# Performance work log

Measured on AMD Instinct MI355X. Metric: run time of the kernel, lower is better.

## Reference

```python
import jax, jax.numpy as jnp
import numpy as np

N_NODES = 100000
D = 128
N_EDGES = 640000


def _spmm(edge_index, w, x, n):
    # out[i] = sum over edges (i<-j): w * x[j]
    src, dst = edge_index[0], edge_index[1]
    return jax.ops.segment_sum(w[:, None] * x[dst], src, num_segments=n)


def setup_inputs() -> dict:
    key = jax.random.key(0)
    ks = jax.random.split(key, 8)
    inp = {
        "index_vectors": jax.random.normal(ks[0], (N_NODES, D), dtype=jnp.float32),
        "edge_index1": jax.random.randint(ks[1], (2, N_EDGES), 0, N_NODES, dtype=jnp.int64),
        "w1": jnp.ones((N_EDGES,), dtype=jnp.float32),
        "edge_index2": jax.random.randint(ks[2], (2, N_EDGES), 0, N_NODES, dtype=jnp.int64),
        "w2": jnp.ones((N_EDGES,), dtype=jnp.float32),
        "edge_index3": jax.random.randint(ks[3], (2, N_EDGES), 0, N_NODES, dtype=jnp.int64),
        "w3": jnp.ones((N_EDGES,), dtype=jnp.float32),
        "zeroth": jax.random.uniform(ks[4], (1, 1), dtype=jnp.float32),
        "fst": jax.random.uniform(ks[5], (1, 1), dtype=jnp.float32),
        "snd": jax.random.uniform(ks[6], (1, 1), dtype=jnp.float32),
        "trd": jax.random.uniform(ks[7], (1, 1), dtype=jnp.float32),
    }
    return inp


def reference(index_vectors, edge_index1, w1, edge_index2, w2, edge_index3, w3,
              zeroth, fst, snd, trd):
    n = index_vectors.shape[0]
    # hop-1 context: A @ x
    fst_ctx = _spmm(edge_index1, w1, index_vectors, n)
    # hop-2 context: A^2 @ roll(x, 1, axis=1)   (permute_vecs=True)
    snd_ctx = _spmm(edge_index2, w2, jnp.roll(index_vectors, 1, axis=1), n)
    # hop-3 context: A^3 @ roll(x, 2, axis=1)
    trd_ctx = _spmm(edge_index3, w3, jnp.roll(index_vectors, 2, axis=1), n)

    # relu-normalized scalar order weights (get_orders)
    r0, r1, r2, r3 = (jax.nn.relu(zeroth), jax.nn.relu(fst),
                      jax.nn.relu(snd), jax.nn.relu(trd))
    tot = r0 + r1 + r2 + r3 + 1e-6
    r0, r1, r2, r3 = r0 / tot, r1 / tot, r2 / tot, r3 / tot

    # use_sign=False -> plain weighted combination
    return r0 * index_vectors + r1 * fst_ctx + r2 * snd_ctx + r3 * trd_ctx
```

## Files before the change

kernel.cpp:

```cpp
#include <hip/hip_runtime.h>

#define N_NODES 100000
#define D 128
#define N_EDGES 640000
#define TOT_EDGES (3 * N_EDGES)

#define NB   1024
#define NPB  98
#define BCAP 2304
#define RPT  9
#define OVF_CAP 16384
#define NKEY 512

#define EPBA 2560
#define SETBLKA (N_EDGES / EPBA)
#define BLKA (3 * SETBLKA)
#define EPT2 (EPBA / 256)

#define CAST_BLOCKS ((N_NODES * D / 4 + 255) / 256)

#define WS_OVFCNT 0
#define WS_CNT    64
#define WS_TOT    3072064
#define WS_OVF    3076160
#define WS_TMP    3338304
#define WS_OFFS   22212672
#define WS_CNTS   22612672
#define WS_XB     23012672
#define WS_TOTAL_FAST 48612672

#ifndef __has_builtin
#define __has_builtin(x) 0
#endif
#if __has_builtin(__builtin_amdgcn_alignbit)
#define ALIGN16(hi, lo) __builtin_amdgcn_alignbit((hi), (lo), 16)
#else
#define ALIGN16(hi, lo) (((hi) << 16) | ((lo) >> 16))
#endif

__device__ __forceinline__ void load_r(const float* z0, const float* z1,
                                       const float* z2, const float* z3,
                                       float& r0, float& r1, float& r2, float& r3) {
    r0 = fmaxf(z0[0], 0.0f);
    r1 = fmaxf(z1[0], 0.0f);
    r2 = fmaxf(z2[0], 0.0f);
    r3 = fmaxf(z3[0], 0.0f);
    float inv = 1.0f / (r0 + r1 + r2 + r3 + 1e-6f);
    r0 *= inv; r1 *= inv; r2 *= inv; r3 *= inv;
}

__device__ __forceinline__ unsigned short bf16rn(float f) {
    unsigned int u = __float_as_uint(f);
    u += 0x7FFFu + ((u >> 16) & 1u);
    return (unsigned short)(u >> 16);
}

__global__ __launch_bounds__(256) void cast_kernel(const float* __restrict__ x,
                                                   ushort* __restrict__ xb) {
    int i = blockIdx.x * 256 + threadIdx.x;
    if (i >= N_NODES * D / 4) return;
    float4 v = ((const float4*)x)[i];
    ushort4 h;
    h.x = bf16rn(v.x); h.y = bf16rn(v.y); h.z = bf16rn(v.z); h.w = bf16rn(v.w);
    ((ushort4*)xb)[i] = h;
}

__global__ __launch_bounds__(256) void histA_kernel(
        const int* __restrict__ ei1, const int* __restrict__ ei2,
        const int* __restrict__ ei3, int* __restrict__ counts) {
    __shared__ int h[NB];
    int t = threadIdx.x;
    int blk = blockIdx.x;
    for (int i = t; i < NB; i += 256) h[i] = 0;
    __syncthreads();
    int set = blk / SETBLKA;
    int e0  = (blk - set * SETBLKA) * EPBA;
    const int* ei = (set == 0) ? ei1 : (set == 1) ? ei2 : ei3;
    for (int i = t; i < EPBA; i += 256) {
        atomicAdd(&h[ei[e0 + i] / NPB], 1);
    }
    __syncthreads();
    for (int i = t; i < NB; i += 256) counts[blk * NB + i] = h[i];
}

__global__ __launch_bounds__(256) void scanA_kernel(int* __restrict__ counts,
                                                    int* __restrict__ totals) {
    int b = blockIdx.x * 256 + threadIdx.x;
    int run = 0;
    for (int blk = 0; blk < BLKA; ++blk) {
        int c = counts[blk * NB + b];
        counts[blk * NB + b] = run;
        run += c;
    }
    totals[b] = run;
}

__global__ __launch_bounds__(256) void placeA_kernel(
        const int* __restrict__ ei1, const float* __restrict__ w1,
        const int* __restrict__ ei2, const float* __restrict__ w2,
        const int* __restrict__ ei3, const float* __restrict__ w3,
        const float* __restrict__ z0, const float* __restrict__ z1,
        const float* __restrict__ z2, const float* __restrict__ z3,
        const int* __restrict__ bbase,
        int* __restrict__ ovf_count, int4* __restrict__ ovf,
        int2* __restrict__ tmp) {
    __shared__ int bb[NB];
    __shared__ int h[NB];
    __shared__ int ts[256];
    __shared__ int2 srec[EPBA];
    __shared__ int gx[EPBA];

    int t = threadIdx.x;
    int blk = blockIdx.x;
    for (int i = t; i < NB; i += 256) { bb[i] = bbase[blk * NB + i]; h[i] = 0; }
    __syncthreads();

    int set = blk / SETBLKA;
    int e0  = (blk - set * SETBLKA) * EPBA;
    const int* ei;  const float* w;  float rk;
    float r0, r1, r2, r3;
    load_r(z0, z1, z2, z3, r0, r1, r2, r3);
    if      (set == 0) { ei = ei1; w = w1; rk = r1; }
    else if (set == 1) { ei = ei2; w = w2; rk = r2; }
    else               { ei = ei3; w = w3; rk = r3; }

    int bkt[EPT2], rnk[EPT2], lcl[EPT2], dstv[EPT2];
    float scv[EPT2];
#pragma unroll
    for (int k = 0; k < EPT2; ++k) {
        int idx = e0 + t + k * 256;
        int src = ei[idx];
        dstv[k] = ei[N_EDGES + idx];
        scv[k]  = rk * w[idx];
        int b = src / NPB;
        bkt[k] = b;
        lcl[k] = src - b * NPB;
        rnk[k] = atomicAdd(&h[b], 1);
    }
    __syncthreads();

    int loc[4];
    int tot = 0;
#pragma unroll
    for (int k = 0; k < 4; ++k) { loc[k] = tot; tot += h[4 * t + k]; }
    ts[t] = tot;
    __syncthreads();
    for (int off = 1; off < 256; off <<= 1) {
        int v = (t >= off) ? ts[t - off] : 0;
        __syncthreads();
        ts[t] += v;
        __syncthreads();
    }
    int tb = ts[t] - tot;
    __syncthreads();
#pragma unroll
    for (int k = 0; k < 4; ++k) h[4 * t + k] = tb + loc[k];
    __syncthreads();

#pragma unroll
    for (int k = 0; k < EPT2; ++k) {
        int b = bkt[k];
        int s = h[b] + rnk[k];
        int rx = dstv[k] | (set << 17) | (lcl[k] << 19);
        srec[s] = make_int2(rx, __float_as_int(scv[k]));
        int p = bb[b] + rnk[k];
        if (p < BCAP) {
            gx[s] = b * BCAP + p;
        } else {
            gx[s] = -1;
            int o = atomicAdd(ovf_count, 1);
            if (o < OVF_CAP) ovf[o] = make_int4(b * NPB + lcl[k],
                                               dstv[k] | (set << 17),
                                               __float_as_int(scv[k]), 0);
        }
    }
    __syncthreads();

    for (int s = t; s < EPBA; s += 256) {
        int g = gx[s];
        if (g >= 0) tmp[g] = srec[s];
    }
}

__global__ __launch_bounds__(256) void binB_kernel(
        const int* __restrict__ totals, int2* __restrict__ tmp,
        int* __restrict__ offs, int* __restrict__ cnts) {
    __shared__ int dH[NKEY];
    __shared__ int ts[256];
    __shared__ int cur[NKEY];
    __shared__ int nb[NPB + 1];
    int b = blockIdx.x;
    int t = threadIdx.x;
    int n = totals[b];
    if (n > BCAP) n = BCAP;

    int mrx[RPT], mry[RPT];
#pragma unroll
    for (int k = 0; k < RPT; ++k) {
        int i = t + k * 256;
        if (i < n) { int2 r = tmp[(size_t)b * BCAP + i]; mrx[k] = r.x; mry[k] = r.y; }
        else       { mrx[k] = -1; mry[k] = 0; }
    }

    dH[t] = 0; dH[t + 256] = 0;
    __syncthreads();
#pragma unroll
    for (int k = 0; k < RPT; ++k) {
        if (mrx[k] != -1) {
            int key = (((mrx[k] >> 19) & 0x7F) << 2) | ((mrx[k] >> 17) & 3);
            atomicAdd(&dH[key], 1);
        }
    }
    __syncthreads();

    int k0 = dH[2 * t], k1 = dH[2 * t + 1];
    int tot = k0 + k1;
    ts[t] = tot;
    __syncthreads();
    for (int off = 1; off < 256; off <<= 1) {
        int v = (t >= off) ? ts[t - off] : 0;
        __syncthreads();
        ts[t] += v;
        __syncthreads();
    }
    int tb = ts[t] - tot;
    cur[2 * t]     = tb;
    cur[2 * t + 1] = tb + k0;
    __syncthreads();

    if (t <= NPB) nb[t] = (t < NPB) ? cur[t << 2] : n;
    __syncthreads();

#pragma unroll
    for (int k = 0; k < RPT; ++k) {
        if (mrx[k] != -1) {
            int key = (((mrx[k] >> 19) & 0x7F) << 2) | ((mrx[k] >> 17) & 3);
            int pos = atomicAdd(&cur[key], 1);
            tmp[(size_t)b * BCAP + pos] = make_int2(mrx[k], mry[k]);
        }
    }

    if (t < NPB) {
        int node = b * NPB + t;
        if (node < N_NODES) {
            offs[node] = b * BCAP + nb[t];
            cnts[node] = nb[t + 1] - nb[t];
        }
    }
}

#define GB_ACCUM(RX, RY)                                                       \
    {                                                                          \
        const uint4* rowp = (const uint4*)(xb + (size_t)((RX) & 0x1FFFF) * D); \
        uint4 v = rowp[l16];                                                   \
        int sh = ((RX) >> 17) & 3;                                             \
        float sc = __int_as_float(RY);                                         \
        unsigned int pw = (unsigned int)__shfl((int)v.w, prevq);               \
        unsigned int s1x = ALIGN16(v.x, pw);                                   \
        unsigned int s1y = ALIGN16(v.y, v.x);                                  \
        unsigned int s1z = ALIGN16(v.z, v.y);                                  \
        unsigned int s1w = ALIGN16(v.w, v.z);                                  \
        unsigned int u0 = (sh == 0) ? v.x : (sh == 1) ? s1x : pw;              \
        unsigned int u1 = (sh == 0) ? v.y : (sh == 1) ? s1y : v.x;             \
        unsigned int u2 = (sh == 0) ? v.z : (sh == 1) ? s1z : v.y;             \
        unsigned int u3 = (sh == 0) ? v.w : (sh == 1) ? s1w : v.z;             \
        acc0 += sc * __uint_as_float(u0 << 16);                                \
        acc1 += sc * __uint_as_float(u0 & 0xFFFF0000u);                        \
        acc2 += sc * __uint_as_float(u1 << 16);                                \
        acc3 += sc * __uint_as_float(u1 & 0xFFFF0000u);                        \
        acc4 += sc * __uint_as_float(u2 << 16);                                \
        acc5 += sc * __uint_as_float(u2 & 0xFFFF0000u);                        \
        acc6 += sc * __uint_as_float(u3 << 16);                                \
        acc7 += sc * __uint_as_float(u3 & 0xFFFF0000u);                        \
    }

__global__ __launch_bounds__(256) void gatherb_kernel(
        const float* __restrict__ x, const ushort* __restrict__ xb,
        const int* __restrict__ offs, const int* __restrict__ cnts,
        const int2* __restrict__ recs,
        const float* __restrict__ z0, const float* __restrict__ z1,
        const float* __restrict__ z2, const float* __restrict__ z3,
        float* __restrict__ out) {
    int wid  = (blockIdx.x * blockDim.x + threadIdx.x) >> 6;
    int lane = threadIdx.x & 63;
    if (wid >= N_NODES) return;

    float r0, r1, r2, r3;
    load_r(z0, z1, z2, z3, r0, r1, r2, r3);

    int qt    = lane >> 4;
    int l16   = lane & 15;
    int prevq = (qt << 4) | ((l16 + 15) & 15);

    int beg   = offs[wid];
    int count = cnts[wid];
    int cnt64 = (count < 64) ? count : 64;

    int mrx = 0, mry = 0;
    if (lane < cnt64) { int2 rec = recs[beg + lane]; mrx = rec.x; mry = rec.y; }

    float acc0 = 0.f, acc1 = 0.f, acc2 = 0.f, acc3 = 0.f;
    float acc4 = 0.f, acc5 = 0.f, acc6 = 0.f, acc7 = 0.f;

    for (int j = 0; j < cnt64; j += 4) {
        int srcl = j + qt;
        int rx = __shfl(mrx, srcl);
        int ry = __shfl(mry, srcl);
        GB_ACCUM(rx, ry)
    }
    for (int q = 64; q < count; q += 4) {
        int qq = q + qt;
        int rx = 0, ry = 0;
        if (qq < count) { int2 rec = recs[beg + qq]; rx = rec.x; ry = rec.y; }
        GB_ACCUM(rx, ry)
    }

    acc0 += __shfl_xor(acc0, 16); acc0 += __shfl_xor(acc0, 32);
    acc1 += __shfl_xor(acc1, 16); acc1 += __shfl_xor(acc1, 32);
    acc2 += __shfl_xor(acc2, 16); acc2 += __shfl_xor(acc2, 32);
    acc3 += __shfl_xor(acc3, 16); acc3 += __shfl_xor(acc3, 32);
    acc4 += __shfl_xor(acc4, 16); acc4 += __shfl_xor(acc4, 32);
    acc5 += __shfl_xor(acc5, 16); acc5 += __shfl_xor(acc5, 32);
    acc6 += __shfl_xor(acc6, 16); acc6 += __shfl_xor(acc6, 32);
    acc7 += __shfl_xor(acc7, 16); acc7 += __shfl_xor(acc7, 32);

    if (lane < 16) {
        const float4* xr = (const float4*)(x + (size_t)wid * D);
        float4 xlo = xr[2 * l16];
        float4 xhi = xr[2 * l16 + 1];
        float4 olo, ohi;
        olo.x = r0 * xlo.x + acc0;
        olo.y = r0 * xlo.y + acc1;
        olo.z = r0 * xlo.z + acc2;
        olo.w = r0 * xlo.w + acc3;
        ohi.x = r0 * xhi.x + acc4;
        ohi.y = r0 * xhi.y + acc5;
        ohi.z = r0 * xhi.z + acc6;
        ohi.w = r0 * xhi.w + acc7;
        float4* op = (float4*)(out + (size_t)wid * D);
        op[2 * l16]     = olo;
        op[2 * l16 + 1] = ohi;
    }
}

__global__ void ovf_kernel(const float* __restrict__ x,
                           const int* __restrict__ ovf_count,
                           const int4* __restrict__ ovf,
                           float* __restrict__ out) {
    int total_waves = (gridDim.x * blockDim.x) >> 6;
    int gw   = (blockIdx.x * blockDim.x + threadIdx.x) >> 6;
    int lane = threadIdx.x & 63;
    int n = *ovf_count;
    if (n > OVF_CAP) n = OVF_CAP;
    for (int r = gw; r < n; r += total_waves) {
        int4 rec = ovf[r];
        int src = rec.x;
        int dst = rec.y & 0x1FFFF;
        int sh  = (rec.y >> 17) & 3;
        float sc = __int_as_float(rec.z);
        const float* xr = x + (size_t)dst * D;
        float* orow = out + (size_t)src * D;
        int c0 = 2 * lane, c1 = 2 * lane + 1;
        atomicAdd(&orow[c0], sc * xr[(c0 - sh) & 127]);
        atomicAdd(&orow[c1], sc * xr[(c1 - sh) & 127]);
    }
}

#define SCAN_BLOCKS ((N_NODES + 255) / 256)
#define WS_COUNTS   0
#define WS_OFFSETS  400000
#define WS_CURSORS  800008
#define WS_BSUM     1200008
#define WS_BPRE     1201576
#define WS_RECS     1203144
#define WS_NEEDED_MID (WS_RECS + (size_t)TOT_EDGES * 8)

__global__ void hist_kernel(const int* __restrict__ ei1, const int* __restrict__ ei2,
                            const int* __restrict__ ei3, int* __restrict__ counts) {
    int e = blockIdx.x * blockDim.x + threadIdx.x;
    if (e >= TOT_EDGES) return;
    int set = e / N_EDGES;
    int idx = e - set * N_EDGES;
    const int* ei = (set == 0) ? ei1 : (set == 1) ? ei2 : ei3;
    atomicAdd(&counts[ei[idx]], 1);
}

__global__ void scan1_kernel(const int* __restrict__ counts,
                             int* __restrict__ offsets, int* __restrict__ bsum) {
    __shared__ int s[256];
    int t = threadIdx.x;
    int i = blockIdx.x * 256 + t;
    int v = (i < N_NODES) ? counts[i] : 0;
    s[t] = v;
    __syncthreads();
    for (int off = 1; off < 256; off <<= 1) {
        int u = (t >= off) ? s[t - off] : 0;
        __syncthreads();
        s[t] += u;
        __syncthreads();
    }
    if (i < N_NODES) offsets[i] = s[t] - v;
    if (t == 255) bsum[blockIdx.x] = s[255];
}

__global__ void scan2_kernel(const int* __restrict__ bsum, int* __restrict__ bpre) {
    __shared__ int s[512];
    int t = threadIdx.x;
    int v = (t < SCAN_BLOCKS) ? bsum[t] : 0;
    s[t] = v;
    __syncthreads();
    for (int off = 1; off < 512; off <<= 1) {
        int u = (t >= off) ? s[t - off] : 0;
        __syncthreads();
        s[t] += u;
        __syncthreads();
    }
    if (t < SCAN_BLOCKS) bpre[t] = s[t] - v;
}

__global__ void scan3_kernel(int* __restrict__ offsets, const int* __restrict__ bpre,
                             int* __restrict__ cursors) {
    int i = blockIdx.x * 256 + threadIdx.x;
    if (i < N_NODES) {
        int v = offsets[i] + bpre[blockIdx.x];
        offsets[i] = v;
        cursors[i] = v;
    }
    if (i == 0) offsets[N_NODES] = TOT_EDGES;
}

__global__ void fill_kernel(const int* __restrict__ ei1, const float* __restrict__ w1,
                            const int* __restrict__ ei2, const float* __restrict__ w2,
                            const int* __restrict__ ei3, const float* __restrict__ w3,
                            const float* __restrict__ z0, const float* __restrict__ z1,
                            const float* __restrict__ z2, const float* __restrict__ z3,
                            int* __restrict__ cursors, int2* __restrict__ recs) {
    int e = blockIdx.x * blockDim.x + threadIdx.x;
    if (e >= TOT_EDGES) return;
    int set = e / N_EDGES;
    int idx = e - set * N_EDGES;
    const int* ei;  const float* w;
    if      (set == 0) { ei = ei1; w = w1; }
    else if (set == 1) { ei = ei2; w = w2; }
    else               { ei = ei3; w = w3; }
    float r0, r1, r2, r3;
    load_r(z0, z1, z2, z3, r0, r1, r2, r3);
    float rk = (set == 0) ? r1 : (set == 1) ? r2 : r3;
    int src = ei[idx];
    int dst = ei[N_EDGES + idx];
    float scale = rk * w[idx];
    int pos = atomicAdd(&cursors[src], 1);
    recs[pos] = make_int2(dst | (set << 17), __float_as_int(scale));
}

__global__ void gatherd_kernel(const float* __restrict__ x,
                               const int* __restrict__ offsets,
                               const int2* __restrict__ recs,
                               const float* __restrict__ z0, const float* __restrict__ z1,
                               const float* __restrict__ z2, const float* __restrict__ z3,
                               float* __restrict__ out) {
    int wid  = (blockIdx.x * blockDim.x + threadIdx.x) >> 6;
    int lane = threadIdx.x & 63;
    if (wid >= N_NODES) return;
    float r0, r1, r2, r3;
    load_r(z0, z1, z2, z3, r0, r1, r2, r3);
    float2 xv = ((const float2*)(x + (size_t)wid * D))[lane];
    int beg = offsets[wid];
    int end = offsets[wid + 1];
    float2 a0 = {0.f, 0.f}, a1 = {0.f, 0.f}, a2 = {0.f, 0.f};
    for (int j = beg; j < end; ++j) {
        int2 rec = recs[j];
        float2 v = ((const float2*)(x + (size_t)(rec.x & 0x1FFFF) * D))[lane];
        int sh = (rec.x >> 17) & 3;
        float sc = __int_as_float(rec.y);
        if      (sh == 0) { a0.x += sc * v.x; a0.y += sc * v.y; }
        else if (sh == 1) { a1.x += sc * v.x; a1.y += sc * v.y; }
        else               { a2.x += sc * v.x; a2.y += sc * v.y; }
    }
    int prev = (lane + 63) & 63;
    float r1y = __shfl(a1.y, prev);
    float r2x = __shfl(a2.x, prev);
    float r2y = __shfl(a2.y, prev);
    float2 o;
    o.x = r0 * xv.x + a0.x + r1y  + r2x;
    o.y = r0 * xv.y + a0.y + a1.x + r2y;
    ((float2*)(out + (size_t)wid * D))[lane] = o;
}

extern "C" void kernel_launch(void* const* d_in, const int* in_sizes, int n_in,
                              void* d_out, int out_size, void* d_ws, size_t ws_size,
                              hipStream_t stream) {
    const float* x   = (const float*)d_in[0];
    const int*   ei1 = (const int*)  d_in[1];
    const float* w1  = (const float*)d_in[2];
    const int*   ei2 = (const int*)  d_in[3];
    const float* w2  = (const float*)d_in[4];
    const int*   ei3 = (const int*)  d_in[5];
    const float* w3  = (const float*)d_in[6];
    const float* z0  = (const float*)d_in[7];
    const float* z1  = (const float*)d_in[8];
    const float* z2  = (const float*)d_in[9];
    const float* z3  = (const float*)d_in[10];
    float* out = (float*)d_out;
    char* wsc = (char*)d_ws;

    if (ws_size >= WS_TOTAL_FAST) {
        int*    ovf_count = (int*)   (wsc + WS_OVFCNT);
        int*    counts    = (int*)   (wsc + WS_CNT);
        int*    totals    = (int*)   (wsc + WS_TOT);
        int4*   ovf       = (int4*)  (wsc + WS_OVF);
        int2*   tmp       = (int2*)  (wsc + WS_TMP);
        int*    offs      = (int*)   (wsc + WS_OFFS);
        int*    cnts      = (int*)   (wsc + WS_CNTS);
        ushort* xb        = (ushort*)(wsc + WS_XB);

        hipMemsetAsync(wsc, 0, 64, stream);
        cast_kernel<<<CAST_BLOCKS, 256, 0, stream>>>(x, xb);
        histA_kernel<<<BLKA, 256, 0, stream>>>(ei1, ei2, ei3, counts);
        scanA_kernel<<<4, 256, 0, stream>>>(counts, totals);
        placeA_kernel<<<BLKA, 256, 0, stream>>>(ei1, w1, ei2, w2, ei3, w3,
                                                z0, z1, z2, z3,
                                                counts, ovf_count, ovf, tmp);
        binB_kernel<<<NB, 256, 0, stream>>>(totals, tmp, offs, cnts);
        gatherb_kernel<<<(N_NODES * 64 + 255) / 256, 256, 0, stream>>>(
            x, xb, offs, cnts, tmp, z0, z1, z2, z3, out);
        ovf_kernel<<<128, 256, 0, stream>>>(x, ovf_count, ovf, out);
    } else {
        int*  counts  = (int*) (wsc + WS_COUNTS);
        int*  offsets = (int*) (wsc + WS_OFFSETS);
        int*  cursors = (int*) (wsc + WS_CURSORS);
        int*  bsum    = (int*) (wsc + WS_BSUM);
        int*  bpre    = (int*) (wsc + WS_BPRE);
        int2* recs    = (int2*)(wsc + WS_RECS);

        hipMemsetAsync(counts, 0, N_NODES * sizeof(int), stream);
        hist_kernel<<<TOT_EDGES / 256, 256, 0, stream>>>(ei1, ei2, ei3, counts);
        scan1_kernel<<<SCAN_BLOCKS, 256, 0, stream>>>(counts, offsets, bsum);
        scan2_kernel<<<1, 512, 0, stream>>>(bsum, bpre);
        scan3_kernel<<<SCAN_BLOCKS, 256, 0, stream>>>(offsets, bpre, cursors);
        fill_kernel<<<TOT_EDGES / 256, 256, 0, stream>>>(ei1, w1, ei2, w2, ei3, w3,
                                                         z0, z1, z2, z3, cursors, recs);
        gatherd_kernel<<<(N_NODES * 64 + 255) / 256, 256, 0, stream>>>(x, offsets, recs,
                                                                       z0, z1, z2, z3, out);
    }
}
```

Before: 296.6 us.

## Replace histogram+scan bucket placement with global atomic cursors and fuse cast

Removes the separate histogram and column-scan kernels. Each placement block now reserves its per-bucket slots by calling atomicAdd on padded global cursors, and the bf16 cast of x runs as extra blocks inside the same launch. This cuts two kernel launches, one full pass over the edge indices and the serial 750-block scan. In exchange, the order of records inside each bucket is no longer deterministic, and there are 1024 contended global atomics per block. The workspace memset grows to cover the cursors.

```diff
diff --git a/kernel.cpp b/kernel.cpp
--- a/kernel.cpp
+++ b/kernel.cpp
@@ -20,14 +20,13 @@
 #define CAST_BLOCKS ((N_NODES * D / 4 + 255) / 256)
 
 #define WS_OVFCNT 0
-#define WS_CNT    64
-#define WS_TOT    3072064
-#define WS_OVF    3076160
-#define WS_TMP    3338304
-#define WS_OFFS   22212672
-#define WS_CNTS   22612672
-#define WS_XB     23012672
-#define WS_TOTAL_FAST 48612672
+#define WS_BCUR   64
+#define WS_OVF    65600
+#define WS_TMP    327744
+#define WS_OFFS   19202112
+#define WS_CNTS   19602112
+#define WS_XB     20002112
+#define WS_TOTAL_FAST 45602112
 
 #ifndef __has_builtin
 #define __has_builtin(x) 0
@@ -55,55 +54,26 @@
     return (unsigned short)(u >> 16);
 }
 
-__global__ __launch_bounds__(256) void cast_kernel(const float* __restrict__ x,
-                                                   ushort* __restrict__ xb) {
-    int i = blockIdx.x * 256 + threadIdx.x;
-    if (i >= N_NODES * D / 4) return;
-    float4 v = ((const float4*)x)[i];
-    ushort4 h;
-    h.x = bf16rn(v.x); h.y = bf16rn(v.y); h.z = bf16rn(v.z); h.w = bf16rn(v.w);
-    ((ushort4*)xb)[i] = h;
-}
-
-__global__ __launch_bounds__(256) void histA_kernel(
-        const int* __restrict__ ei1, const int* __restrict__ ei2,
-        const int* __restrict__ ei3, int* __restrict__ counts) {
-    __shared__ int h[NB];
-    int t = threadIdx.x;
-    int blk = blockIdx.x;
-    for (int i = t; i < NB; i += 256) h[i] = 0;
-    __syncthreads();
-    int set = blk / SETBLKA;
-    int e0  = (blk - set * SETBLKA) * EPBA;
-    const int* ei = (set == 0) ? ei1 : (set == 1) ? ei2 : ei3;
-    for (int i = t; i < EPBA; i += 256) {
-        atomicAdd(&h[ei[e0 + i] / NPB], 1);
-    }
-    __syncthreads();
-    for (int i = t; i < NB; i += 256) counts[blk * NB + i] = h[i];
-}
-
-__global__ __launch_bounds__(256) void scanA_kernel(int* __restrict__ counts,
-                                                    int* __restrict__ totals) {
-    int b = blockIdx.x * 256 + threadIdx.x;
-    int run = 0;
-    for (int blk = 0; blk < BLKA; ++blk) {
-        int c = counts[blk * NB + b];
-        counts[blk * NB + b] = run;
-        run += c;
-    }
-    totals[b] = run;
-}
-
-__global__ __launch_bounds__(256) void placeA_kernel(
+__global__ __launch_bounds__(256) void prep_kernel(
+        const float* __restrict__ x, ushort* __restrict__ xb,
         const int* __restrict__ ei1, const float* __restrict__ w1,
         const int* __restrict__ ei2, const float* __restrict__ w2,
         const int* __restrict__ ei3, const float* __restrict__ w3,
         const float* __restrict__ z0, const float* __restrict__ z1,
         const float* __restrict__ z2, const float* __restrict__ z3,
-        const int* __restrict__ bbase,
-        int* __restrict__ ovf_count, int4* __restrict__ ovf,
-        int2* __restrict__ tmp) {
+        int* __restrict__ bcur, int* __restrict__ ovf_count,
+        int4* __restrict__ ovf, int2* __restrict__ tmp) {
+    if (blockIdx.x >= BLKA) {
+        int i = (blockIdx.x - BLKA) * 256 + threadIdx.x;
+        if (i < N_NODES * D / 4) {
+            float4 v = ((const float4*)x)[i];
+            ushort4 h4;
+            h4.x = bf16rn(v.x); h4.y = bf16rn(v.y);
+            h4.z = bf16rn(v.z); h4.w = bf16rn(v.w);
+            ((ushort4*)xb)[i] = h4;
+        }
+        return;
+    }
     __shared__ int bb[NB];
     __shared__ int h[NB];
     __shared__ int ts[256];
@@ -112,14 +82,15 @@
 
     int t = threadIdx.x;
     int blk = blockIdx.x;
-    for (int i = t; i < NB; i += 256) { bb[i] = bbase[blk * NB + i]; h[i] = 0; }
-    __syncthreads();
+    for (int i = t; i < NB; i += 256) h[i] = 0;
+    __syncthreads();
+
+    float r0, r1, r2, r3;
+    load_r(z0, z1, z2, z3, r0, r1, r2, r3);
 
     int set = blk / SETBLKA;
     int e0  = (blk - set * SETBLKA) * EPBA;
     const int* ei;  const float* w;  float rk;
-    float r0, r1, r2, r3;
-    load_r(z0, z1, z2, z3, r0, r1, r2, r3);
     if      (set == 0) { ei = ei1; w = w1; rk = r1; }
     else if (set == 1) { ei = ei2; w = w2; rk = r2; }
     else               { ei = ei3; w = w3; rk = r3; }
@@ -143,6 +114,10 @@
     int tot = 0;
 #pragma unroll
     for (int k = 0; k < 4; ++k) { loc[k] = tot; tot += h[4 * t + k]; }
+    for (int i = t; i < NB; i += 256) {
+        int c = h[i];
+        bb[i] = c ? atomicAdd(&bcur[i * 16], c) : 0;
+    }
     ts[t] = tot;
     __syncthreads();
     for (int off = 1; off < 256; off <<= 1) {
@@ -183,7 +158,7 @@
 }
 
 __global__ __launch_bounds__(256) void binB_kernel(
-        const int* __restrict__ totals, int2* __restrict__ tmp,
+        const int* __restrict__ bcur, int2* __restrict__ tmp,
         int* __restrict__ offs, int* __restrict__ cnts) {
     __shared__ int dH[NKEY];
     __shared__ int ts[256];
@@ -191,7 +166,7 @@
     __shared__ int nb[NPB + 1];
     int b = blockIdx.x;
     int t = threadIdx.x;
-    int n = totals[b];
+    int n = bcur[b * 16];
     if (n > BCAP) n = BCAP;
 
     int mrx[RPT], mry[RPT];
@@ -506,22 +481,18 @@
 
     if (ws_size >= WS_TOTAL_FAST) {
         int*    ovf_count = (int*)   (wsc + WS_OVFCNT);
-        int*    counts    = (int*)   (wsc + WS_CNT);
-        int*    totals    = (int*)   (wsc + WS_TOT);
+        int*    bcur      = (int*)   (wsc + WS_BCUR);
         int4*   ovf       = (int4*)  (wsc + WS_OVF);
         int2*   tmp       = (int2*)  (wsc + WS_TMP);
         int*    offs      = (int*)   (wsc + WS_OFFS);
         int*    cnts      = (int*)   (wsc + WS_CNTS);
         ushort* xb        = (ushort*)(wsc + WS_XB);
 
-        hipMemsetAsync(wsc, 0, 64, stream);
-        cast_kernel<<<CAST_BLOCKS, 256, 0, stream>>>(x, xb);
-        histA_kernel<<<BLKA, 256, 0, stream>>>(ei1, ei2, ei3, counts);
-        scanA_kernel<<<4, 256, 0, stream>>>(counts, totals);
-        placeA_kernel<<<BLKA, 256, 0, stream>>>(ei1, w1, ei2, w2, ei3, w3,
-                                                z0, z1, z2, z3,
-                                                counts, ovf_count, ovf, tmp);
-        binB_kernel<<<NB, 256, 0, stream>>>(totals, tmp, offs, cnts);
+        hipMemsetAsync(wsc, 0, WS_OVF, stream);
+        prep_kernel<<<BLKA + CAST_BLOCKS, 256, 0, stream>>>(
+            x, xb, ei1, w1, ei2, w2, ei3, w3, z0, z1, z2, z3,
+            bcur, ovf_count, ovf, tmp);
+        binB_kernel<<<NB, 256, 0, stream>>>(bcur, tmp, offs, cnts);
         gatherb_kernel<<<(N_NODES * 64 + 255) / 256, 256, 0, stream>>>(
             x, xb, offs, cnts, tmp, z0, z1, z2, z3, out);
         ovf_kernel<<<128, 256, 0, stream>>>(x, ovf_count, ovf, out);
```

After: 286.8 us. -3.3%, faster.
